# Performance work log

Measured on AMD Instinct MI355X. Metric: run time of the kernel, lower is better.

The kernel has to match this reference:

```python
import jax, jax.numpy as jnp
import numpy as np

B, TE, TD = 16, 400, 64
E, H = 256, 512
H2 = 2 * H  # 1024
V = 32000


def setup_inputs():
    key = jax.random.key(0)
    k = jax.random.split(key, 16)
    s = 0.05
    return {
        "encoder_inputs": jax.random.randint(k[0], (B, TE), 0, V),
        "decoder_inputs": jax.random.randint(k[1], (B, TD), 0, V),
        "ext_oov_sizes": jax.random.randint(k[2], (B,), 0, 10),
        "enc_idxes_on_ext_voc": jax.random.randint(k[3], (B, TE), 0, V),
        "h0": jnp.zeros((2, B, H), jnp.float32),
        "c0": jnp.zeros((2, B, H), jnp.float32),
        "emb": jax.random.normal(k[4], (V, E)) * 0.1,
        "Wih_f": jax.random.normal(k[5], (4 * H, E)) * s,
        "Whh_f": jax.random.normal(k[6], (4 * H, H)) * s,
        "b_f": jnp.zeros((4 * H,), jnp.float32),
        "Wih_b": jax.random.normal(k[7], (4 * H, E)) * s,
        "Whh_b": jax.random.normal(k[8], (4 * H, H)) * s,
        "b_b": jnp.zeros((4 * H,), jnp.float32),
        "Wih_d": jax.random.normal(k[9], (4 * H2, E + 2 * H2)) * s,
        "Whh_d": jax.random.normal(k[10], (4 * H2, H2)) * s,
        "b_d": jnp.zeros((4 * H2,), jnp.float32),
        "W_ea": jax.random.normal(k[11], (H2, H2)) * 0.006,
        "W_da": jax.random.normal(k[12], (H2, H2)) * 0.006,
        "W_v": jax.random.normal(k[13], (V, 3 * H2)) * s,
        "b_v": jnp.zeros((V,), jnp.float32),
    }


def lstm_cell(x, h, c, Wih, Whh, b):
    z = x @ Wih.T + h @ Whh.T + b
    i, f, g, o = jnp.split(z, 4, axis=-1)
    i, f, o = jax.nn.sigmoid(i), jax.nn.sigmoid(f), jax.nn.sigmoid(o)
    c2 = f * c + i * jnp.tanh(g)
    return o * jnp.tanh(c2), c2


def run_lstm(xs, h0, c0, Wih, Whh, b):
    # xs: [T, B, E]
    def step(carry, x):
        h, c = lstm_cell(x, carry[0], carry[1], Wih, Whh, b)
        return (h, c), h
    (h, c), hs = jax.lax.scan(step, (h0, c0), xs)
    return hs, h, c


def _forward(emb, Wih_f, Whh_f, b_f, Wih_b, Whh_b, b_b, Wih_d, Whh_d, b_d,
             W_ea, W_da, W_v, b_v, h0, c0, encoder_inputs, decoder_inputs):
    xs = emb[encoder_inputs].transpose(1, 0, 2)  # [TE, B, E]
    hs_f, hf, cf = run_lstm(xs, h0[0], c0[0], Wih_f, Whh_f, b_f)
    hs_b, hb, cb = run_lstm(xs[::-1], h0[1], c0[1], Wih_b, Whh_b, b_b)
    enc_out = jnp.concatenate([hs_f, hs_b[::-1]], axis=-1).transpose(1, 0, 2)  # [B, TE, 2H]
    h = jnp.concatenate([hf, hb], axis=-1)  # [B, 2H] (torch reshape of bi-dir last hidden)
    c = jnp.concatenate([cf, cb], axis=-1)
    dec_emb = emb[decoder_inputs].transpose(1, 0, 2)  # [TD, B, E]

    def step(carry, xs_t):
        h, c, accum, buf = carry
        i, emb_t = xs_t
        # intra-temporal encoder attention: exp scores normalized by past accumulation
        scores = jnp.einsum('bd,btd->bt', h @ W_ea, enc_out)  # [B, TE]
        exp_s = jnp.exp(scores)
        denom = jnp.where(i == 0, jnp.ones_like(accum), accum)
        ep = exp_s / denom
        attn = ep / jnp.sum(ep, axis=-1, keepdims=True)
        ctx_e = jnp.einsum('bt,btd->bd', attn, enc_out)
        # intra-decoder attention over previously produced hidden states (masked)
        dsc = jnp.einsum('bd,tbd->bt', h @ W_da, buf)  # [B, TD]
        dsc = jnp.where((jnp.arange(TD) < i)[None, :], dsc, -1e30)
        dw = jnp.where(i == 0, 0.0, jax.nn.softmax(dsc, axis=-1))
        ctx_d = jnp.einsum('bt,tbd->bd', dw, buf)
        x = jnp.concatenate([emb_t, ctx_e, ctx_d], axis=-1)  # [B, E+4H]
        h2, c2 = lstm_cell(x, h, c, Wih_d, Whh_d, b_d)
        buf2 = buf.at[i].set(h2)
        feat = jnp.concatenate([h2, ctx_e, ctx_d], axis=-1)  # [B, 6H]
        logd = jax.nn.log_softmax(feat @ W_v.T + b_v, axis=-1)
        return (h2, c2, accum + exp_s, buf2), logd

    carry0 = (h, c, jnp.zeros((B, TE), h.dtype), jnp.zeros((TD, B, H2), h.dtype))
    (h, c, _, _), logds = jax.lax.scan(step, carry0, (jnp.arange(TD), dec_emb))
    return logds.transpose(1, 0, 2), h[None], c[None]


def reference(encoder_inputs, decoder_inputs, ext_oov_sizes, enc_idxes_on_ext_voc,
              h0, c0, emb, Wih_f, Whh_f, b_f, Wih_b, Whh_b, b_b,
              Wih_d, Whh_d, b_d, W_ea, W_da, W_v, b_v):
    # ext_oov_sizes / enc_idxes_on_ext_voc are unused by forward (as in the torch source)
    return _forward(emb, Wih_f, Whh_f, b_f, Wih_b, Whh_b, b_b, Wih_d, Whh_d, b_d,
                    W_ea, W_da, W_v, b_v, h0, c0, encoder_inputs, decoder_inputs)
```

## Files before the change

kernel.cpp:

```cpp
#include <hip/hip_runtime.h>
#include <math.h>

#define B_  16
#define TE_ 400
#define TD_ 64
#define E_  256
#define H_  512
#define H2_ 1024
#define V_  32000

typedef __attribute__((ext_vector_type(4))) float f32x4;
typedef __attribute__((ext_vector_type(8))) short s16x8;
typedef __attribute__((ext_vector_type(8))) unsigned short u16x8;
typedef __attribute__((ext_vector_type(4))) unsigned short u16x4;

__device__ __forceinline__ float bf2f(unsigned short u){
  union { unsigned int i; float f; } v; v.i = ((unsigned int)u) << 16; return v.f;
}
__device__ __forceinline__ unsigned short f2bf(float f){
  union { float f; unsigned int i; } v; v.f = f;
  return (unsigned short)((v.i + 0x7fffu + ((v.i >> 16) & 1u)) >> 16);
}
__device__ __forceinline__ float sigmoidf_(float x){ return 1.f/(1.f + expf(-x)); }

__device__ __forceinline__ void gl_lds16(const void* gsrc, void* ldst){
  __builtin_amdgcn_global_load_lds(
      (const __attribute__((address_space(1))) unsigned int*)gsrc,
      (__attribute__((address_space(3))) unsigned int*)ldst, 16, 0, 0);
}

__device__ __forceinline__ void arrive8(unsigned* inst){
  __threadfence();
  __hip_atomic_fetch_add(inst + (blockIdx.x & 7u)*16, 1u, __ATOMIC_RELAXED, __HIP_MEMORY_SCOPE_AGENT);
}
__device__ __forceinline__ void poll8(unsigned* inst, unsigned target){
  int it = 0;
  for(;;){
    unsigned s = 0;
    #pragma unroll
    for (int k = 0; k < 8; ++k)
      s += __hip_atomic_load(inst + k*16, __ATOMIC_RELAXED, __HIP_MEMORY_SCOPE_AGENT);
    if (s >= target) break;
    if (it < 6) __builtin_amdgcn_s_sleep(1);
    else if (it < 24) __builtin_amdgcn_s_sleep(4);
    else __builtin_amdgcn_s_sleep(16);
    ++it;
  }
}

__global__ void k_init(unsigned* bars, float* ctxn, float* psumT){
  int gid = blockIdx.x*256 + threadIdx.x;
  if (gid < 81920) bars[gid] = 0u;
  if (gid < 32768) ctxn[gid] = 0.f;
  if (gid < 32) psumT[gid] = 0.f;
}

__global__ void k_gather(const float* __restrict__ emb, const int* __restrict__ idx,
                         unsigned short* __restrict__ out, int T){
  int wv = threadIdx.x >> 6, l = threadIdx.x & 63;
  int row = blockIdx.x*4 + wv;
  if (row >= T*B_) return;
  int t = row >> 4, b = row & 15;
  int tok = idx[b*T + t];
  float4 v = *(const float4*)(emb + (size_t)tok*E_ + l*4);
  u16x4 o; o[0]=f2bf(v.x); o[1]=f2bf(v.y); o[2]=f2bf(v.z); o[3]=f2bf(v.w);
  *(u16x4*)(out + (size_t)row*E_ + l*4) = o;
}

__global__ void k_prep_enc(const float* __restrict__ Wih_f, const float* __restrict__ Whh_f,
                           const float* __restrict__ Wih_b, const float* __restrict__ Whh_b,
                           unsigned short* __restrict__ Wenc){
  int it = blockIdx.x*256 + threadIdx.x;
  int dir = it / (2048*96); int rem = it % (2048*96);
  int pr = rem / 96; int kc = rem % 96; int k0 = kc*8;
  int g = pr >> 6, r = pr & 63, gate = r >> 4, ul = r & 15;
  int orig = gate*H_ + g*16 + ul;
  const float* Wih = dir ? Wih_b : Wih_f;
  const float* Whh = dir ? Whh_b : Whh_f;
  u16x8 o;
  #pragma unroll
  for (int e = 0; e < 8; ++e){
    int k = k0 + e;
    float v = (k < E_) ? Wih[(size_t)orig*E_ + k] : Whh[(size_t)orig*H_ + (k - E_)];
    o[e] = f2bf(v);
  }
  *(u16x8*)(Wenc + ((size_t)dir*2048 + pr)*768 + k0) = o;
}

__device__ __forceinline__ void prep_whext_item(int it, const float* __restrict__ Whh_d,
                                                const float* __restrict__ W_da,
                                                char* __restrict__ WhExt){
  if (it < 524288){
    int g = it >> 13; int rem = it & 8191;
    int kblk = rem >> 10; int rem2 = rem & 1023;
    int row = rem2 >> 4; int k8 = rem2 & 15;
    int gate = row >> 4, ul = row & 15;
    int orig = gate*H2_ + g*16 + ul;
    u16x8 o;
    #pragma unroll
    for (int e = 0; e < 8; ++e)
      o[e] = f2bf(Whh_d[(size_t)orig*H2_ + kblk*128 + k8*8 + e]);
    size_t off = (size_t)g*163840 + (size_t)kblk*20480 + (size_t)(row*256 + ((k8*16) ^ ((row&7)<<4)));
    *(u16x8*)(WhExt + off) = o;
  } else if (it < 655360){
    int qi = it - 524288;
    int g = qi >> 11; int rem = qi & 2047;
    int kblk = rem >> 8; int c2 = rem & 255;
    int wvv = c2 >> 6, rr = (c2 >> 2) & 15, c = c2 & 3;
    int row = g*16 + rr;
    u16x8 o;
    #pragma unroll
    for (int e = 0; e < 8; ++e)
      o[e] = f2bf(W_da[(size_t)row*H2_ + kblk*128 + wvv*32 + c*8 + e]);
    size_t off = (size_t)g*163840 + (size_t)kblk*20480 + 16384
               + (size_t)(wvv*1024 + rr*64 + ((c*16) ^ ((rr&3)<<4)));
    *(u16x8*)(WhExt + off) = o;
  }
}

__device__ __forceinline__ void prep_ctx_item(int it, const float* __restrict__ Wih_d,
                                              char* __restrict__ CtxW){
  int g = it >> 14; int rem = it & 16383;
  int kblk = rem >> 10; int rem2 = rem & 1023;
  int row = rem2 >> 4; int k8 = rem2 & 15;
  int gate = row >> 4, ul = row & 15;
  int orig = gate*H2_ + g*16 + ul;
  int k = 256 + kblk*128 + k8*8;
  u16x8 o;
  #pragma unroll
  for (int e = 0; e < 8; ++e)
    o[e] = f2bf(Wih_d[(size_t)orig*2304 + k + e]);
  size_t off = (size_t)g*262144 + (size_t)kblk*16384 + (size_t)(row*256 + ((k8*16) ^ ((row&7)<<4)));
  *(u16x8*)(CtxW + off) = o;
}

__global__ void k_prep_wihemb(const float* __restrict__ Wih_d, unsigned short* __restrict__ Wemb){
  int it = blockIdx.x*256 + threadIdx.x;
  int p = it >> 5; int k0 = (it & 31)*8;
  int g = p >> 6, gate = (p >> 4) & 3, ul = p & 15;
  int orig = gate*H2_ + g*16 + ul;
  u16x8 o;
  #pragma unroll
  for (int e = 0; e < 8; ++e)
    o[e] = f2bf(Wih_d[(size_t)orig*2304 + k0 + e]);
  *(u16x8*)(Wemb + (size_t)p*256 + k0) = o;
}

__global__ void __launch_bounds__(256, 2) k_zinit(
    const unsigned short* __restrict__ A,
    const unsigned short* __restrict__ Bw,
    const float* __restrict__ bd,
    float* __restrict__ Cz)
{
  __shared__ unsigned short Ab[128*72];
  __shared__ unsigned short Bt[128*72];
  int p = blockIdx.x;
  int mt = p >> 5, nt = p & 31;
  int m0 = mt*128, n0 = nt*128;
  int tid = threadIdx.x, wvv = tid>>6, l = tid&63;
  int wr = wvv>>1, wc = wvv&1;
  f32x4 zero4 = {0.f,0.f,0.f,0.f};
  f32x4 acc[4][4];
  #pragma unroll
  for (int a=0;a<4;++a){
    #pragma unroll
    for (int b=0;b<4;++b) acc[a][b] = zero4;
  }
  for (int k0 = 0; k0 < 256; k0 += 64){
    #pragma unroll
    for (int qq = 0; qq < 4; ++qq){
      int idx8 = (tid + qq*256)*8;
      int r = idx8 >> 6, k = idx8 & 63;
      *(u16x8*)(Ab + r*72 + k) = *(const u16x8*)(A + (size_t)(m0+r)*256 + k0 + k);
      *(u16x8*)(Bt + r*72 + k) = *(const u16x8*)(Bw + (size_t)(n0+r)*256 + k0 + k);
    }
    __syncthreads();
    #pragma unroll
    for (int ks = 0; ks < 2; ++ks){
      s16x8 af[4], bf[4];
      #pragma unroll
      for (int fi=0;fi<4;++fi)
        af[fi] = *(const s16x8*)(Ab + (wr*64+fi*16+(l&15))*72 + ks*32 + (l>>4)*8);
      #pragma unroll
      for (int fj=0;fj<4;++fj)
        bf[fj] = *(const s16x8*)(Bt + (wc*64+fj*16+(l&15))*72 + ks*32 + (l>>4)*8);
      #pragma unroll
      for (int fi=0;fi<4;++fi){
        #pragma unroll
        for (int fj=0;fj<4;++fj)
          acc[fi][fj] = __builtin_amdgcn_mfma_f32_16x16x32_bf16(af[fi], bf[fj], acc[fi][fj], 0,0,0);
      }
    }
    __syncthreads();
  }
  #pragma unroll
  for (int fj=0;fj<4;++fj){
    int col = n0 + wc*64 + fj*16 + (l&15);
    int orig = ((col>>4)&3)*H2_ + (col>>6)*16 + (col&15);
    float bias = bd[orig];
    #pragma unroll
    for (int fi=0;fi<4;++fi){
      #pragma unroll
      for (int j=0;j<4;++j){
        int row = m0 + wr*64 + fi*16 + (l>>4)*4 + j;
        Cz[(size_t)row*4096 + col] = acc[fi][fj][j] + bias;
      }
    }
  }
}

__global__ void __launch_bounds__(256, 2) k_zx(
    const unsigned short* __restrict__ xs,
    const unsigned short* __restrict__ Wenc,
    const float* __restrict__ b_f, const float* __restrict__ b_b,
    unsigned short* __restrict__ zx)
{
  __shared__ unsigned short Ab[128*72];
  __shared__ unsigned short Bt[128*72];
  int pblk = blockIdx.x;
  int dir = pblk / 800; int rem = pblk % 800;
  int mt = rem >> 4, nt = rem & 15;
  int m0 = mt*128, n0 = nt*128;
  int tid = threadIdx.x, wvv = tid>>6, l = tid&63;
  int wr = wvv>>1, wc = wvv&1;
  f32x4 zero4 = {0.f,0.f,0.f,0.f};
  f32x4 acc[4][4];
  #pragma unroll
  for (int a=0;a<4;++a){
    #pragma unroll
    for (int b=0;b<4;++b) acc[a][b] = zero4;
  }
  for (int k0 = 0; k0 < 256; k0 += 64){
    #pragma unroll
    for (int qq = 0; qq < 4; ++qq){
      int idx8 = (tid + qq*256)*8;
      int r = idx8 >> 6, k = idx8 & 63;
      *(u16x8*)(Ab + r*72 + k) = *(const u16x8*)(xs + (size_t)(m0+r)*256 + k0 + k);
      *(u16x8*)(Bt + r*72 + k) = *(const u16x8*)(Wenc + ((size_t)dir*2048 + n0+r)*768 + k0 + k);
    }
    __syncthreads();
    #pragma unroll
    for (int ks = 0; ks < 2; ++ks){
      s16x8 af[4], bf[4];
      #pragma unroll
      for (int fi=0;fi<4;++fi)
        af[fi] = *(const s16x8*)(Ab + (wr*64+fi*16+(l&15))*72 + ks*32 + (l>>4)*8);
      #pragma unroll
      for (int fj=0;fj<4;++fj)
        bf[fj] = *(const s16x8*)(Bt + (wc*64+fj*16+(l&15))*72 + ks*32 + (l>>4)*8);
      #pragma unroll
      for (int fi=0;fi<4;++fi){
        #pragma unroll
        for (int fj=0;fj<4;++fj)
          acc[fi][fj] = __builtin_amdgcn_mfma_f32_16x16x32_bf16(af[fi], bf[fj], acc[fi][fj], 0,0,0);
      }
    }
    __syncthreads();
  }
  const float* bsrc = dir ? b_b : b_f;
  #pragma unroll
  for (int fj=0;fj<4;++fj){
    int col = n0 + wc*64 + fj*16 + (l&15);
    float bias = bsrc[((col>>4)&3)*512 + (col>>6)*16 + (col&15)];
    #pragma unroll
    for (int fi=0;fi<4;++fi){
      #pragma unroll
      for (int j=0;j<4;++j){
        int row = m0 + wr*64 + fi*16 + (l>>4)*4 + j;
        zx[((size_t)dir*6400 + row)*2048 + col] = f2bf(acc[fi][fj][j] + bias);
      }
    }
  }
}

__global__ void __launch_bounds__(256, 2) k_penc(
    const unsigned short* __restrict__ enc,
    const float* __restrict__ Wea,
    unsigned short* __restrict__ P)
{
  __shared__ unsigned short Ab[128*72];
  __shared__ unsigned short Bt[128*72];
  int p = blockIdx.x;
  int mt = p >> 3, nt = p & 7;
  int m0 = mt*128, n0 = nt*128;
  int tid = threadIdx.x, wvv = tid>>6, l = tid&63;
  int wr = wvv>>1, wc = wvv&1;
  f32x4 zero4 = {0.f,0.f,0.f,0.f};
  f32x4 acc[4][4];
  #pragma unroll
  for (int a=0;a<4;++a){
    #pragma unroll
    for (int b=0;b<4;++b) acc[a][b] = zero4;
  }
  for (int k0 = 0; k0 < 1024; k0 += 64){
    #pragma unroll
    for (int qq = 0; qq < 4; ++qq){
      int idx8 = (tid + qq*256)*8;
      int r = idx8 >> 6, k = idx8 & 63;
      *(u16x8*)(Ab + r*72 + k) = *(const u16x8*)(enc + (size_t)(m0+r)*1024 + k0 + k);
    }
    #pragma unroll
    for (int qq = 0; qq < 4; ++qq){
      int idx8 = (tid + qq*256)*8;
      int r = idx8 >> 6, k = idx8 & 63;
      const float* src = Wea + (size_t)(n0+r)*1024 + k0 + k;
      float4 v0 = *(const float4*)src;
      float4 v1 = *(const float4*)(src+4);
      u16x8 o;
      o[0]=f2bf(v0.x); o[1]=f2bf(v0.y); o[2]=f2bf(v0.z); o[3]=f2bf(v0.w);
      o[4]=f2bf(v1.x); o[5]=f2bf(v1.y); o[6]=f2bf(v1.z); o[7]=f2bf(v1.w);
      *(u16x8*)(Bt + r*72 + k) = o;
    }
    __syncthreads();
    #pragma unroll
    for (int ks = 0; ks < 2; ++ks){
      s16x8 af[4], bf[4];
      #pragma unroll
      for (int fi=0;fi<4;++fi)
        af[fi] = *(const s16x8*)(Ab + (wr*64+fi*16+(l&15))*72 + ks*32 + (l>>4)*8);
      #pragma unroll
      for (int fj=0;fj<4;++fj)
        bf[fj] = *(const s16x8*)(Bt + (wc*64+fj*16+(l&15))*72 + ks*32 + (l>>4)*8);
      #pragma unroll
      for (int fi=0;fi<4;++fi){
        #pragma unroll
        for (int fj=0;fj<4;++fj)
          acc[fi][fj] = __builtin_amdgcn_mfma_f32_16x16x32_bf16(af[fi], bf[fj], acc[fi][fj], 0,0,0);
      }
    }
    __syncthreads();
  }
  #pragma unroll
  for (int fj=0;fj<4;++fj){
    int col = n0 + wc*64 + fj*16 + (l&15);
    #pragma unroll
    for (int fi=0;fi<4;++fi){
      #pragma unroll
      for (int j=0;j<4;++j){
        int row = m0 + wr*64 + fi*16 + (l>>4)*4 + j;
        P[(size_t)row*1024 + col] = f2bf(acc[fi][fj][j]);
      }
    }
  }
}

__global__ void __launch_bounds__(256, 1) k_encoder(
    const unsigned short* __restrict__ zx,
    const unsigned short* __restrict__ Wenc,
    const float* __restrict__ h0, const float* __restrict__ c0,
    unsigned short* __restrict__ enc_out,
    unsigned short* __restrict__ hbuf,
    float* __restrict__ h0dec, float* __restrict__ c0dec,
    unsigned* __restrict__ bars,
    const float* __restrict__ Whh_d, const float* __restrict__ W_da,
    const float* __restrict__ Wih_d,
    char* __restrict__ WhExt, char* __restrict__ CtxW)
{
  extern __shared__ char smem[];
  int tid = threadIdx.x;
  int w = blockIdx.x;
  if (w >= 64){
    int base = (w - 64)*256 + tid;
    for (int it = base; it < 655360; it += 36864) prep_whext_item(it, Whh_d, W_da, WhExt);
    for (int it = base; it < 1048576; it += 36864) prep_ctx_item(it, Wih_d, CtxW);
    return;
  }
  unsigned short* Wt = (unsigned short*)smem;
  unsigned short* At = Wt + 64*520;
  float* zl = (float*)(At + 16*520);
  int dir = w >> 5, g = w & 31;
  int wv = tid >> 6, l = tid & 63;
  {
    const unsigned short* Wsrc = Wenc + ((size_t)dir*2048 + g*64)*768 + 256;
    int r = tid >> 2, s = tid & 3;
    for (int c = 0; c < 16; ++c)
      *(u16x8*)(Wt + r*520 + s*128 + c*8) = *(const u16x8*)(Wsrc + (size_t)r*768 + s*128 + c*8);
  }
  int bb = tid >> 4, ul = tid & 15;
  float creg = c0[((size_t)dir*16 + bb)*H_ + g*16 + ul];
  int kchunk = (l >> 4) * 8;
  f32x4 zero4 = { 0.f, 0.f, 0.f, 0.f };
  {
    int r = tid >> 4, s = tid & 15;
    for (int e = 0; e < 32; ++e)
      At[r*520 + s*32 + e] = f2bf(h0[((size_t)dir*16 + r)*H_ + s*32 + e]);
  }
  int tg0 = dir ? (TE_-1) : 0;
  const unsigned short* zrow = zx + ((size_t)dir*6400 + (size_t)tg0*16 + (l>>4)*4)*2048 + g*64 + wv*16 + (l&15);
  f32x4 a0cur;
  a0cur[0]=bf2f(zrow[0]); a0cur[1]=bf2f(zrow[2048]); a0cur[2]=bf2f(zrow[4096]); a0cur[3]=bf2f(zrow[6144]);
  __syncthreads();
  for (int t = 0; t < TE_; ++t){
    int tg = dir ? (TE_-1 - t) : t;
    f32x4 acc0 = a0cur, acc1 = zero4;
    const unsigned short* brow = Wt + (wv*16 + (l&15))*520 + kchunk;
    const unsigned short* ap   = At + (l&15)*520 + kchunk;
    #pragma unroll
    for (int ks = 0; ks < 16; ++ks){
      s16x8 afr = *(const s16x8*)(ap + ks*32);
      s16x8 bfr = *(const s16x8*)(brow + ks*32);
      if (ks & 1) acc1 = __builtin_amdgcn_mfma_f32_16x16x32_bf16(afr, bfr, acc1, 0, 0, 0);
      else        acc0 = __builtin_amdgcn_mfma_f32_16x16x32_bf16(afr, bfr, acc0, 0, 0, 0);
    }
    f32x4 acc = acc0 + acc1;
    #pragma unroll
    for (int j = 0; j < 4; ++j)
      zl[wv*256 + ((l>>4)*4 + j)*16 + (l&15)] = acc[j];
    __syncthreads();
    float zi = zl[0*256 + bb*16 + ul];
    float zf = zl[1*256 + bb*16 + ul];
    float zg = zl[2*256 + bb*16 + ul];
    float zo = zl[3*256 + bb*16 + ul];
    float iv = sigmoidf_(zi), fv = sigmoidf_(zf), gv = tanhf(zg), ov = sigmoidf_(zo);
    float cc = fv*creg + iv*gv;
    float hh = ov * tanhf(cc);
    creg = cc;
    int u = g*16 + ul;
    unsigned short hb = f2bf(hh);
    hbuf[((size_t)dir*2 + ((t+1)&1))*(16*H_) + bb*H_ + u] = hb;
    enc_out[((size_t)bb*TE_ + tg)*H2_ + dir*H_ + u] = hb;
    if (t == TE_-1){
      h0dec[(size_t)bb*H2_ + dir*H_ + u] = hh;
      c0dec[(size_t)bb*H2_ + dir*H_ + u] = cc;
    }
    unsigned* cnt = bars + (size_t)(dir*400 + t)*64;
    __syncthreads();
    if (tid == 0){
      __threadfence();
      __hip_atomic_fetch_add(cnt + (g&3)*16, 1u, __ATOMIC_RELAXED, __HIP_MEMORY_SCOPE_AGENT);
    }
    if (t+1 < TE_){
      int tg2 = dir ? (TE_-2 - t) : (t+1);
      const unsigned short* zr2 = zx + ((size_t)dir*6400 + (size_t)tg2*16 + (l>>4)*4)*2048 + g*64 + wv*16 + (l&15);
      a0cur[0]=bf2f(zr2[0]); a0cur[1]=bf2f(zr2[2048]); a0cur[2]=bf2f(zr2[4096]); a0cur[3]=bf2f(zr2[6144]);
    }
    if (tid == 0){
      int it = 0;
      for(;;){
        unsigned s_ = 0;
        #pragma unroll
        for (int k2 = 0; k2 < 4; ++k2)
          s_ += __hip_atomic_load(cnt + k2*16, __ATOMIC_RELAXED, __HIP_MEMORY_SCOPE_AGENT);
        if (s_ >= 32) break;
        if (it < 6) __builtin_amdgcn_s_sleep(1);
        else __builtin_amdgcn_s_sleep(4);
        ++it;
      }
      __threadfence();
    }
    __syncthreads();
    if (t+1 < TE_){
      int r = tid >> 4, s = tid & 15;
      const unsigned short* hsrc = hbuf + ((size_t)dir*2 + ((t+1)&1))*(16*H_) + r*H_ + s*32;
      for (int c = 0; c < 4; ++c)
        *(u16x8*)(At + r*520 + s*32 + c*8) = *(const u16x8*)(hsrc + c*8);
    }
    __syncthreads();
  }
}

__global__ void k_dec_init(const float* __restrict__ h0dec, unsigned short* __restrict__ hreg){
  int gid = blockIdx.x*256 + threadIdx.x;
  if (gid < 16384) hreg[gid] = f2bf(h0dec[gid]);
}

__device__ __forceinline__ void issueA(const char* gA, char* BbA, int wv, int l, int kblk, int buf){
  const char* gsrc = gA + (size_t)kblk*20480;
  char* lb = BbA + buf*20480;
  #pragma unroll
  for (int q = 0; q < 4; ++q)
    gl_lds16(gsrc + wv*4096 + q*1024 + (size_t)l*16, lb + wv*4096 + q*1024);
  gl_lds16(gsrc + 16384 + wv*1024 + (size_t)l*16, lb + 16384 + wv*1024);
}
__device__ __forceinline__ void issueC(const char* gC, char* BbC, int wv, int l, int kblk, int buf){
  const char* gsrc = gC + (size_t)kblk*16384;
  char* lb = BbC + buf*16384;
  #pragma unroll
  for (int q = 0; q < 4; ++q)
    gl_lds16(gsrc + wv*4096 + q*1024 + (size_t)l*16, lb + wv*4096 + q*1024);
}

__global__ void __launch_bounds__(256, 1) k_decoder(
  const char* __restrict__ WhExt,
  const char* __restrict__ CtxW,
  const float* __restrict__ zinit,
  const unsigned short* __restrict__ Penc,
  const unsigned short* __restrict__ enc_out,
  const float* __restrict__ c0dec,
  unsigned short* __restrict__ hreg,
  unsigned short* __restrict__ xbuf,
  float* __restrict__ ctxn,
  float* __restrict__ psumT,
  unsigned short* __restrict__ vbuf,
  unsigned short* __restrict__ bufh,
  unsigned short* __restrict__ Av,
  float* __restrict__ outHC,
  unsigned* __restrict__ bars)
{
  extern __shared__ char smem[];
  int tid = threadIdx.x, w = blockIdx.x;
  int wv = tid >> 6, l = tid & 63;
  unsigned* dbase = bars + 51200;

  unsigned short* Atc = (unsigned short*)smem;
  unsigned short* Ah  = (unsigned short*)smem;
  char* BbA = smem + 66560;
  char* BbC = smem + 128000;
  float* zq = (float*)(smem + 66560);
  float* zl = (float*)(smem + 128000);
  unsigned short* encL = (unsigned short*)smem;
  float* epL  = (float*)(smem + 103424);
  float* accL = (float*)(smem + 103680);
  float* dscL = (float*)smem;

  bool isZ = (w < 64);
  bool isE = (w >= 64 && w < 192);
  int eb = 0, ec = 0;
  if (isE){ eb = (w-64) >> 3; ec = (w-64) & 7; }
  int db = w - 192;

  if (isE){
    for (int rr = 0; rr < 50; ++rr){
      const unsigned short* src = enc_out + ((size_t)eb*TE_ + ec*50 + rr)*H2_;
      *(u16x4*)(encL + rr*1032 + tid*4) = *(const u16x4*)(src + tid*4);
    }
    if (tid < 50) accL[tid] = 0.f;
    __syncthreads();
  }
  float creg = 0.f;
  int bb = tid >> 4, ul = tid & 15;
  const char* gA = WhExt + (size_t)w*163840;
  const char* gC = CtxW + (size_t)w*262144;
  f32x4 acc0, acc1;

  for (int i = 0; i < TD_; ++i){
    int p = i & 1;
    unsigned* barM = dbase + (size_t)(i*3+0)*128;
    unsigned* barA = dbase + (size_t)(i*3+1)*128;
    unsigned* barB = dbase + (size_t)(i*3+2)*128;

    if (isZ){
      ctxn[(p^1)*16384 + w*256 + tid] = 0.f;
      if (w == 0 && tid < 16) psumT[(p^1)*16 + tid] = 0.f;
      const float* zsrc = zinit + ((size_t)i*16 + (l>>4)*4)*4096 + w*64 + wv*16 + (l&15);
      f32x4 a0i; a0i[0]=zsrc[0]; a0i[1]=zsrc[4096]; a0i[2]=zsrc[8192]; a0i[3]=zsrc[12288];
      issueA(gA, BbA, wv, l, 0, 0);
      issueA(gA, BbA, wv, l, 1, 1);
      {
        int r = tid >> 4, s = tid & 15;
        const unsigned short* hsrc = hreg + p*16384 + r*H2_ + s*64;
        for (int c = 0; c < 8; ++c)
          *(u16x8*)(Ah + r*1032 + s*64 + c*8) = *(const u16x8*)(hsrc + c*8);
      }
      __syncthreads();
      acc0 = a0i;
      f32x4 z4 = {0.f,0.f,0.f,0.f};
      acc1 = z4;
      f32x4 accv = z4;
      int swz = ((l&7)<<4);
      for (int kblk = 0; kblk < 8; ++kblk){
        int buf = kblk % 3;
        if (kblk + 2 < 8) issueA(gA, BbA, wv, l, kblk+2, (kblk+2)%3);
        if (kblk < 6)       asm volatile("s_waitcnt vmcnt(10)" ::: "memory");
        else if (kblk == 6) asm volatile("s_waitcnt vmcnt(5)" ::: "memory");
        else                asm volatile("s_waitcnt vmcnt(0)" ::: "memory");
        const unsigned short* ap = Ah + (l&15)*1032 + kblk*128 + (l>>4)*8;
        const char* Bz = BbA + buf*20480 + wv*4096;
        #pragma unroll
        for (int ks = 0; ks < 4; ++ks){
          int k8 = ks*4 + (l>>4);
          s16x8 afr = *(const s16x8*)(ap + ks*32);
          s16x8 bfr = *(const s16x8*)(Bz + (l&15)*256 + ((k8*16) ^ swz));
          if (ks & 1) acc1 = __builtin_amdgcn_mfma_f32_16x16x32_bf16(afr, bfr, acc1, 0,0,0);
          else        acc0 = __builtin_amdgcn_mfma_f32_16x16x32_bf16(afr, bfr, acc0, 0,0,0);
        }
        s16x8 afq = *(const s16x8*)(Ah + (l&15)*1032 + kblk*128 + wv*32 + (l>>4)*8);
        s16x8 bfv = *(const s16x8*)(BbA + buf*20480 + 16384 + wv*1024 + (l&15)*64 + ((((l>>4)*16)) ^ ((l&3)<<4)));
        accv = __builtin_amdgcn_mfma_f32_16x16x32_bf16(afq, bfv, accv, 0,0,0);
      }
      __syncthreads();
      #pragma unroll
      for (int j = 0; j < 4; ++j)
        zq[wv*256 + ((l>>4)*4+j)*16 + (l&15)] = accv[j];
      __syncthreads();
      if (i > 0){
        float vv = zq[0*256+bb*16+ul] + zq[1*256+bb*16+ul] + zq[2*256+bb*16+ul] + zq[3*256+bb*16+ul];
        vbuf[((size_t)(i-1)*16 + bb)*H2_ + w*16 + ul] = f2bf(vv);
      }
      __syncthreads();
      if (tid == 0) arrive8(barM);
      issueC(gC, BbC, wv, l, 0, 0);
      issueC(gC, BbC, wv, l, 1, 1);
      if (tid == 0){ poll8(barA, 144); __threadfence(); }
      __syncthreads();
      {
        int r = tid >> 4, s = tid & 15;
        float inv = 1.f / psumT[p*16 + r];
        const float* cn = ctxn + p*16384 + (size_t)r*1024 + s*64;
        for (int c8 = 0; c8 < 8; ++c8){
          float4 v0 = *(const float4*)(cn + c8*8);
          float4 v1 = *(const float4*)(cn + c8*8 + 4);
          u16x8 o;
          o[0]=f2bf(v0.x*inv); o[1]=f2bf(v0.y*inv); o[2]=f2bf(v0.z*inv); o[3]=f2bf(v0.w*inv);
          o[4]=f2bf(v1.x*inv); o[5]=f2bf(v1.y*inv); o[6]=f2bf(v1.z*inv); o[7]=f2bf(v1.w*inv);
          *(u16x8*)(Atc + r*2056 + s*64 + c8*8) = o;
        }
        const unsigned short* xd = xbuf + (size_t)r*1024 + s*64;
        for (int c8 = 0; c8 < 8; ++c8)
          *(u16x8*)(Atc + r*2056 + 1024 + s*64 + c8*8) = *(const u16x8*)(xd + c8*8);
      }
      {
        float val = ctxn[p*16384 + (size_t)bb*1024 + w*16 + ul] / psumT[p*16 + bb];
        Av[((size_t)bb*TD_ + i)*3072 + 1024 + w*16 + ul] = f2bf(val);
      }
      __syncthreads();
      for (int k = 0; k < 16; ++k){
        if (k < 15) asm volatile("s_waitcnt vmcnt(4)" ::: "memory");
        else        asm volatile("s_waitcnt vmcnt(0)" ::: "memory");
        const unsigned short* ap = Atc + (l&15)*2056 + k*128 + (l>>4)*8;
        const char* Bz = BbC + (k&1)*16384 + wv*4096;
        #pragma unroll
        for (int ks = 0; ks < 4; ++ks){
          int k8 = ks*4 + (l>>4);
          s16x8 afr = *(const s16x8*)(ap + ks*32);
          s16x8 bfr = *(const s16x8*)(Bz + (l&15)*256 + ((k8*16) ^ swz));
          if (ks & 1) acc1 = __builtin_amdgcn_mfma_f32_16x16x32_bf16(afr, bfr, acc1, 0,0,0);
          else        acc0 = __builtin_amdgcn_mfma_f32_16x16x32_bf16(afr, bfr, acc0, 0,0,0);
        }
        if (k + 2 < 16) issueC(gC, BbC, wv, l, k+2, k&1);
      }
      __syncthreads();
      f32x4 acc = acc0 + acc1;
      #pragma unroll
      for (int j = 0; j < 4; ++j)
        zl[wv*256 + ((l>>4)*4+j)*16 + (l&15)] = acc[j];
      __syncthreads();
      float zi = zl[0*256 + bb*16 + ul];
      float zf = zl[1*256 + bb*16 + ul];
      float zg = zl[2*256 + bb*16 + ul];
      float zo = zl[3*256 + bb*16 + ul];
      if (i == 0) creg = c0dec[(size_t)bb*H2_ + w*16 + ul];
      float iv = sigmoidf_(zi), fv = sigmoidf_(zf), gv = tanhf(zg), ov = sigmoidf_(zo);
      float cc = fv*creg + iv*gv;
      float hh = ov*tanhf(cc);
      creg = cc;
      int u = w*16 + ul;
      unsigned short hb2 = f2bf(hh);
      hreg[((i+1)&1)*16384 + (size_t)bb*H2_ + u] = hb2;
      Av[((size_t)bb*TD_ + i)*3072 + u] = hb2;
      bufh[((size_t)i*16 + bb)*H2_ + u] = hb2;
      if (i == TD_-1){
        outHC[(size_t)bb*H2_ + u] = hh;
        outHC[16384 + (size_t)bb*H2_ + u] = cc;
      }
      __syncthreads();
      if (tid == 0){ arrive8(barB); poll8(barB, 64); __threadfence(); }
      __syncthreads();
    } else if (isE){
      const unsigned short* hb_ = hreg + p*16384 + eb*H2_ + l*16;
      u16x8 hv0 = *(const u16x8*)hb_;
      u16x8 hv1 = *(const u16x8*)(hb_ + 8);
      float hf[16];
      #pragma unroll
      for (int c = 0; c < 8; ++c){ hf[c] = bf2f(hv0[c]); hf[8+c] = bf2f(hv1[c]); }
      for (int rr = wv; rr < 50; rr += 4){
        const unsigned short* pr = Penc + ((size_t)(eb*TE_ + ec*50 + rr))*H2_ + l*16;
        u16x8 p0 = *(const u16x8*)pr;
        u16x8 p1 = *(const u16x8*)(pr + 8);
        float sc = 0.f;
        #pragma unroll
        for (int c = 0; c < 8; ++c) sc += hf[c]*bf2f(p0[c]);
        #pragma unroll
        for (int c = 0; c < 8; ++c) sc += hf[8+c]*bf2f(p1[c]);
        #pragma unroll
        for (int o = 1; o < 64; o <<= 1) sc += __shfl_xor(sc, o);
        if (l == 0){
          float es = expf(sc);
          float aold = accL[rr];
          float denom = (i == 0) ? 1.f : aold;
          accL[rr] = aold + es;
          epL[rr] = es / denom;
        }
      }
      __syncthreads();
      float tot = 0.f;
      for (int rr = 0; rr < 50; ++rr) tot += epL[rr];
      float a0=0.f,a1=0.f,a2=0.f,a3=0.f;
      for (int rr = 0; rr < 50; ++rr){
        float wgt = epL[rr];
        u16x4 ev = *(const u16x4*)(encL + rr*1032 + tid*4);
        a0 += wgt*bf2f(ev[0]); a1 += wgt*bf2f(ev[1]); a2 += wgt*bf2f(ev[2]); a3 += wgt*bf2f(ev[3]);
      }
      float* dst = ctxn + p*16384 + (size_t)eb*1024 + tid*4;
      atomicAdd(dst+0, a0); atomicAdd(dst+1, a1); atomicAdd(dst+2, a2); atomicAdd(dst+3, a3);
      if (tid == 0) atomicAdd(psumT + p*16 + eb, tot);
      __syncthreads();
      if (tid == 0){ arrive8(barA); poll8(barB, 64); __threadfence(); }
      __syncthreads();
    } else {
      int col = tid*4;
      if (i == 0){
        u16x4 z4v = {0,0,0,0};
        *(u16x4*)(xbuf + (size_t)db*1024 + col) = z4v;
        *(u16x4*)(Av + ((size_t)db*TD_ + i)*3072 + 2048 + col) = z4v;
      } else {
        if (tid == 0){ poll8(barM, 64); __threadfence(); }
        __syncthreads();
        const unsigned short* hq = hreg + p*16384 + db*H2_ + l*16;
        u16x8 h0v = *(const u16x8*)hq;
        u16x8 h1v = *(const u16x8*)(hq + 8);
        float qf[16];
        #pragma unroll
        for (int c = 0; c < 8; ++c){ qf[c] = bf2f(h0v[c]); qf[8+c] = bf2f(h1v[c]); }
        for (int tp = wv; tp < i; tp += 4){
          const unsigned short* vr = vbuf + ((size_t)tp*16 + db)*H2_ + l*16;
          u16x8 e0 = *(const u16x8*)vr;
          u16x8 e1 = *(const u16x8*)(vr + 8);
          float sc = 0.f;
          #pragma unroll
          for (int c = 0; c < 8; ++c) sc += qf[c]*bf2f(e0[c]);
          #pragma unroll
          for (int c = 0; c < 8; ++c) sc += qf[8+c]*bf2f(e1[c]);
          #pragma unroll
          for (int o = 1; o < 64; o <<= 1) sc += __shfl_xor(sc, o);
          if (l == 0) dscL[tp] = sc;
        }
        __syncthreads();
        float scv = (l < i) ? dscL[l] : -1e30f;
        float m = scv;
        #pragma unroll
        for (int o = 1; o < 64; o <<= 1) m = fmaxf(m, __shfl_xor(m, o));
        float e = (l < i) ? expf(scv - m) : 0.f;
        float ssum = e;
        #pragma unroll
        for (int o = 1; o < 64; o <<= 1) ssum += __shfl_xor(ssum, o);
        float wgt = e / ssum;
        float c0_=0.f,c1_=0.f,c2_=0.f,c3_=0.f;
        for (int tp = 0; tp < i; ++tp){
          float wt = __shfl(wgt, tp);
          u16x4 hv = *(const u16x4*)(bufh + ((size_t)tp*16 + db)*H2_ + col);
          c0_ += wt*bf2f(hv[0]); c1_ += wt*bf2f(hv[1]); c2_ += wt*bf2f(hv[2]); c3_ += wt*bf2f(hv[3]);
        }
        u16x4 o4; o4[0]=f2bf(c0_); o4[1]=f2bf(c1_); o4[2]=f2bf(c2_); o4[3]=f2bf(c3_);
        *(u16x4*)(xbuf + (size_t)db*1024 + col) = o4;
        *(u16x4*)(Av + ((size_t)db*TD_ + i)*3072 + 2048 + col) = o4;
      }
      __syncthreads();
      if (tid == 0){ arrive8(barA); poll8(barB, 64); __threadfence(); }
      __syncthreads();
    }
  }
}

__global__ void __launch_bounds__(256, 2) k_vocab_gemm(
    const unsigned short* __restrict__ Av,
    const float* __restrict__ Wv,
    const float* __restrict__ bv,
    float* __restrict__ out)
{
  __shared__ unsigned short Ab[128*72];
  __shared__ unsigned short Bt[128*72];
  int p = blockIdx.x;
  int mt = (p>>3)&7, nt = (p&7) + 8*(p>>6);
  if (nt >= 250) return;
  int m0 = mt*128, n0 = nt*128;
  int tid = threadIdx.x, wvv = tid>>6, l = tid&63;
  int wr = wvv>>1, wc = wvv&1;
  f32x4 zero4 = {0.f,0.f,0.f,0.f};
  f32x4 acc[4][4];
  #pragma unroll
  for (int a=0;a<4;++a){
    #pragma unroll
    for (int b=0;b<4;++b) acc[a][b] = zero4;
  }
  for (int k0 = 0; k0 < 3072; k0 += 64){
    #pragma unroll
    for (int qq = 0; qq < 4; ++qq){
      int idx8 = (tid + qq*256)*8;
      int r = idx8 >> 6, k = idx8 & 63;
      *(u16x8*)(Ab + r*72 + k) = *(const u16x8*)(Av + (size_t)(m0+r)*3072 + k0 + k);
    }
    #pragma unroll
    for (int qq = 0; qq < 4; ++qq){
      int idx8 = (tid + qq*256)*8;
      int r = idx8 >> 6, k = idx8 & 63;
      const float* src = Wv + (size_t)(n0+r)*3072 + k0 + k;
      float4 v0 = *(const float4*)src;
      float4 v1 = *(const float4*)(src+4);
      u16x8 o;
      o[0]=f2bf(v0.x); o[1]=f2bf(v0.y); o[2]=f2bf(v0.z); o[3]=f2bf(v0.w);
      o[4]=f2bf(v1.x); o[5]=f2bf(v1.y); o[6]=f2bf(v1.z); o[7]=f2bf(v1.w);
      *(u16x8*)(Bt + r*72 + k) = o;
    }
    __syncthreads();
    #pragma unroll
    for (int ks = 0; ks < 2; ++ks){
      s16x8 af[4], bf[4];
      #pragma unroll
      for (int fi=0;fi<4;++fi)
        af[fi] = *(const s16x8*)(Ab + (wr*64+fi*16+(l&15))*72 + ks*32 + (l>>4)*8);
      #pragma unroll
      for (int fj=0;fj<4;++fj)
        bf[fj] = *(const s16x8*)(Bt + (wc*64+fj*16+(l&15))*72 + ks*32 + (l>>4)*8);
      #pragma unroll
      for (int fi=0;fi<4;++fi){
        #pragma unroll
        for (int fj=0;fj<4;++fj)
          acc[fi][fj] = __builtin_amdgcn_mfma_f32_16x16x32_bf16(af[fi], bf[fj], acc[fi][fj], 0,0,0);
      }
    }
    __syncthreads();
  }
  #pragma unroll
  for (int fj=0;fj<4;++fj){
    int col = n0 + wc*64 + fj*16 + (l&15);
    float bias = bv[col];
    #pragma unroll
    for (int fi=0;fi<4;++fi){
      #pragma unroll
      for (int j=0;j<4;++j){
        int row = m0 + wr*64 + fi*16 + (l>>4)*4 + j;
        out[(size_t)row*V_ + col] = acc[fi][fj][j] + bias;
      }
    }
  }
}

__global__ void k_logsoftmax(float* __restrict__ out){
  int row = blockIdx.x;
  float* x = out + (size_t)row*V_;
  int tid = threadIdx.x;
  __shared__ float red[64];
  float m = -1e30f;
  for (int c = tid; c < V_; c += 256) m = fmaxf(m, x[c]);
  #pragma unroll
  for (int o=1;o<64;o<<=1) m = fmaxf(m, __shfl_xor(m,o));
  if ((tid&63)==0) red[tid>>6] = m;
  __syncthreads();
  m = fmaxf(fmaxf(red[0],red[1]), fmaxf(red[2],red[3]));
  float s = 0.f;
  for (int c = tid; c < V_; c += 256) s += expf(x[c]-m);
  #pragma unroll
  for (int o=1;o<64;o<<=1) s += __shfl_xor(s,o);
  if ((tid&63)==0) red[8 + (tid>>6)] = s;
  __syncthreads();
  s = red[8]+red[9]+red[10]+red[11];
  float lse = m + logf(s);
  for (int c = tid; c < V_; c += 256) x[c] = x[c] - lse;
}

extern "C" void kernel_launch(void* const* d_in, const int* in_sizes, int n_in,
                              void* d_out, int out_size, void* d_ws, size_t ws_size,
                              hipStream_t stream){
  (void)in_sizes; (void)n_in; (void)out_size; (void)ws_size;
  const int*   enc_in = (const int*)d_in[0];
  const int*   dec_in = (const int*)d_in[1];
  const float* h0   = (const float*)d_in[4];
  const float* c0   = (const float*)d_in[5];
  const float* emb  = (const float*)d_in[6];
  const float* Wih_f= (const float*)d_in[7];
  const float* Whh_f= (const float*)d_in[8];
  const float* b_f  = (const float*)d_in[9];
  const float* Wih_b= (const float*)d_in[10];
  const float* Whh_b= (const float*)d_in[11];
  const float* b_b  = (const float*)d_in[12];
  const float* Wih_d= (const float*)d_in[13];
  const float* Whh_d= (const float*)d_in[14];
  const float* b_d  = (const float*)d_in[15];
  const float* W_ea = (const float*)d_in[16];
  const float* W_da = (const float*)d_in[17];
  const float* W_v  = (const float*)d_in[18];
  const float* b_v  = (const float*)d_in[19];
  float* out = (float*)d_out;
  char* ws = (char*)d_ws;

  size_t o_bars   = 0;
  size_t o_ctxn   = 327680;
  size_t o_psumT  = o_ctxn + 131072;
  size_t o_xs     = o_psumT + 256;
  size_t o_decemb = o_xs + (size_t)6400*256*2;
  size_t o_Wenc   = o_decemb + (size_t)1024*256*2;
  size_t o_WhExt  = o_Wenc + (size_t)2*2048*768*2;
  size_t o_CtxW   = o_WhExt + (size_t)64*163840;
  size_t o_Wemb   = o_CtxW + (size_t)64*262144;
  size_t o_zinit  = o_Wemb + (size_t)4096*256*2;
  size_t o_zx     = o_zinit + (size_t)1024*4096*4;
  size_t o_enc    = o_zx + (size_t)2*6400*2048*2;
  size_t o_Penc   = o_enc + (size_t)16*400*1024*2;
  size_t o_hbuf   = o_Penc + (size_t)16*400*1024*2;
  size_t o_h0dec  = o_hbuf + (size_t)2*2*16*512*2;
  size_t o_c0dec  = o_h0dec + (size_t)16*1024*4;
  size_t o_hreg   = o_c0dec + (size_t)16*1024*4;
  size_t o_xbuf   = o_hreg + (size_t)2*16*1024*2;
  size_t o_vbuf   = o_xbuf + (size_t)16*1024*2;
  size_t o_bufh   = o_vbuf + (size_t)64*16*1024*2;
  size_t o_Av     = o_bufh + (size_t)64*16*1024*2;

  unsigned* bars        = (unsigned*)(ws + o_bars);
  float* ctxn           = (float*)(ws + o_ctxn);
  float* psumT          = (float*)(ws + o_psumT);
  unsigned short* xs    = (unsigned short*)(ws + o_xs);
  unsigned short* decemb= (unsigned short*)(ws + o_decemb);
  unsigned short* Wenc  = (unsigned short*)(ws + o_Wenc);
  char* WhExt           = ws + o_WhExt;
  char* CtxW            = ws + o_CtxW;
  unsigned short* Wemb  = (unsigned short*)(ws + o_Wemb);
  float* zinit          = (float*)(ws + o_zinit);
  unsigned short* zx    = (unsigned short*)(ws + o_zx);
  unsigned short* encO  = (unsigned short*)(ws + o_enc);
  unsigned short* Penc  = (unsigned short*)(ws + o_Penc);
  unsigned short* hbuf  = (unsigned short*)(ws + o_hbuf);
  float* h0dec          = (float*)(ws + o_h0dec);
  float* c0dec          = (float*)(ws + o_c0dec);
  unsigned short* hreg  = (unsigned short*)(ws + o_hreg);
  unsigned short* xbuf  = (unsigned short*)(ws + o_xbuf);
  unsigned short* vbuf  = (unsigned short*)(ws + o_vbuf);
  unsigned short* bufh  = (unsigned short*)(ws + o_bufh);
  unsigned short* Av    = (unsigned short*)(ws + o_Av);

  hipFuncSetAttribute((const void*)k_encoder, hipFuncAttributeMaxDynamicSharedMemorySize, 90000);
  hipFuncSetAttribute((const void*)k_decoder, hipFuncAttributeMaxDynamicSharedMemorySize, 160768);

  k_init<<<320, 256, 0, stream>>>(bars, ctxn, psumT);
  k_gather<<<1600, 256, 0, stream>>>(emb, enc_in, xs, TE_);
  k_gather<<<256, 256, 0, stream>>>(emb, dec_in, decemb, TD_);
  k_prep_enc<<<1536, 256, 0, stream>>>(Wih_f, Whh_f, Wih_b, Whh_b, Wenc);
  k_prep_wihemb<<<512, 256, 0, stream>>>(Wih_d, Wemb);
  k_zinit<<<256, 256, 0, stream>>>(decemb, Wemb, b_d, zinit);
  k_zx<<<1600, 256, 0, stream>>>(xs, Wenc, b_f, b_b, zx);
  k_encoder<<<208, 256, 87296, stream>>>(zx, Wenc, h0, c0, encO, hbuf, h0dec, c0dec, bars,
                                         Whh_d, W_da, Wih_d, WhExt, CtxW);
  k_penc<<<400, 256, 0, stream>>>(encO, W_ea, Penc);
  k_dec_init<<<64, 256, 0, stream>>>(h0dec, hreg);
  k_decoder<<<208, 256, 160768, stream>>>(WhExt, CtxW, zinit, Penc, encO, c0dec,
                                          hreg, xbuf, ctxn, psumT, vbuf, bufh, Av,
                                          out + (size_t)32768000, bars);
  k_vocab_gemm<<<2048, 256, 0, stream>>>(Av, W_v, b_v, out);
  k_logsoftmax<<<1024, 256, 0, stream>>>(out);
}
```

Baseline: 5.538 ms.

## Deepen decoder ctx-weight prefetch, hoist A prefetch across barrier, warm L2, relayout barriers

The decoder's context-weight stream now uses a four-deep buffer that borrows the A-weight LDS slots, where it was double-buffered before. The next step's A-weight prefetch is issued before the end-of-step barrier poll instead of at the start of the step. Idle attention blocks read the Z-blocks' weight slices while waiting, to keep them warm in L2. Barrier counters are re-laid out so each per-block-group counter array is contiguous, which needs a larger init region and a shifted workspace offset. The aim is to hide weight-load latency and barrier wait time in the serial decoder loop, at the cost of extra memory traffic and LDS slot aliasing that must stay race-free.

```diff
diff --git a/kernel.cpp b/kernel.cpp
--- a/kernel.cpp
+++ b/kernel.cpp
@@ -29,28 +29,29 @@
       (__attribute__((address_space(3))) unsigned int*)ldst, 16, 0, 0);
 }
 
-__device__ __forceinline__ void arrive8(unsigned* inst){
+__device__ __forceinline__ void d_arrive(unsigned* bars, int inst){
   __threadfence();
-  __hip_atomic_fetch_add(inst + (blockIdx.x & 7u)*16, 1u, __ATOMIC_RELAXED, __HIP_MEMORY_SCOPE_AGENT);
-}
-__device__ __forceinline__ void poll8(unsigned* inst, unsigned target){
+  __hip_atomic_fetch_add(bars + (blockIdx.x & 7u)*4096 + inst*16, 1u, __ATOMIC_RELAXED, __HIP_MEMORY_SCOPE_AGENT);
+}
+__device__ __forceinline__ void d_poll(unsigned* bars, int inst, unsigned tgt){
   int it = 0;
   for(;;){
     unsigned s = 0;
     #pragma unroll
     for (int k = 0; k < 8; ++k)
-      s += __hip_atomic_load(inst + k*16, __ATOMIC_RELAXED, __HIP_MEMORY_SCOPE_AGENT);
-    if (s >= target) break;
+      s += __hip_atomic_load(bars + k*4096 + inst*16, __ATOMIC_RELAXED, __HIP_MEMORY_SCOPE_AGENT);
+    if (s >= tgt) break;
     if (it < 6) __builtin_amdgcn_s_sleep(1);
     else if (it < 24) __builtin_amdgcn_s_sleep(4);
     else __builtin_amdgcn_s_sleep(16);
     ++it;
   }
+  __threadfence();
 }
 
 __global__ void k_init(unsigned* bars, float* ctxn, float* psumT){
   int gid = blockIdx.x*256 + threadIdx.x;
-  if (gid < 81920) bars[gid] = 0u;
+  if (gid < 99328) bars[gid] = 0u;
   if (gid < 32768) ctxn[gid] = 0.f;
   if (gid < 32) psumT[gid] = 0.f;
 }
@@ -370,6 +371,7 @@
   float* zl = (float*)(At + 16*520);
   int dir = w >> 5, g = w & 31;
   int wv = tid >> 6, l = tid & 63;
+  unsigned* ebars = bars + 32768;
   {
     const unsigned short* Wsrc = Wenc + ((size_t)dir*2048 + g*64)*768 + 256;
     int r = tid >> 2, s = tid & 3;
@@ -423,11 +425,11 @@
       h0dec[(size_t)bb*H2_ + dir*H_ + u] = hh;
       c0dec[(size_t)bb*H2_ + dir*H_ + u] = cc;
     }
-    unsigned* cnt = bars + (size_t)(dir*400 + t)*64;
+    int inst = dir*400 + t;
     __syncthreads();
     if (tid == 0){
       __threadfence();
-      __hip_atomic_fetch_add(cnt + (g&3)*16, 1u, __ATOMIC_RELAXED, __HIP_MEMORY_SCOPE_AGENT);
+      __hip_atomic_fetch_add(ebars + (g&3)*16384 + inst*16, 1u, __ATOMIC_RELAXED, __HIP_MEMORY_SCOPE_AGENT);
     }
     if (t+1 < TE_){
       int tg2 = dir ? (TE_-2 - t) : (t+1);
@@ -440,7 +442,7 @@
         unsigned s_ = 0;
         #pragma unroll
         for (int k2 = 0; k2 < 4; ++k2)
-          s_ += __hip_atomic_load(cnt + k2*16, __ATOMIC_RELAXED, __HIP_MEMORY_SCOPE_AGENT);
+          s_ += __hip_atomic_load(ebars + k2*16384 + inst*16, __ATOMIC_RELAXED, __HIP_MEMORY_SCOPE_AGENT);
         if (s_ >= 32) break;
         if (it < 6) __builtin_amdgcn_s_sleep(1);
         else __builtin_amdgcn_s_sleep(4);
@@ -472,9 +474,12 @@
     gl_lds16(gsrc + wv*4096 + q*1024 + (size_t)l*16, lb + wv*4096 + q*1024);
   gl_lds16(gsrc + 16384 + wv*1024 + (size_t)l*16, lb + 16384 + wv*1024);
 }
-__device__ __forceinline__ void issueC(const char* gC, char* BbC, int wv, int l, int kblk, int buf){
+__device__ __forceinline__ char* cslot(char* BbA, char* BbC, int s){
+  if (s < 2) return BbC + s*16384;
+  return BbA + (s-2)*20480;
+}
+__device__ __forceinline__ void issueC(const char* gC, char* lb, int wv, int l, int kblk){
   const char* gsrc = gC + (size_t)kblk*16384;
-  char* lb = BbC + buf*16384;
   #pragma unroll
   for (int q = 0; q < 4; ++q)
     gl_lds16(gsrc + wv*4096 + q*1024 + (size_t)l*16, lb + wv*4096 + q*1024);
@@ -500,7 +505,6 @@
   extern __shared__ char smem[];
   int tid = threadIdx.x, w = blockIdx.x;
   int wv = tid >> 6, l = tid & 63;
-  unsigned* dbase = bars + 51200;
 
   unsigned short* Atc = (unsigned short*)smem;
   unsigned short* Ah  = (unsigned short*)smem;
@@ -531,21 +535,28 @@
   int bb = tid >> 4, ul = tid & 15;
   const char* gA = WhExt + (size_t)w*163840;
   const char* gC = CtxW + (size_t)w*262144;
+  const char* warmbase = 0; int warmhalf4 = 0;
+  if (isE){
+    int j = w - 64;
+    if (j < 64){ warmbase = WhExt + (size_t)j*163840; warmhalf4 = 5120; }
+    else       { warmbase = CtxW + (size_t)(j-64)*262144; warmhalf4 = 8192; }
+  }
   f32x4 acc0, acc1;
+
+  if (isZ){
+    issueA(gA, BbA, wv, l, 0, 0);
+    issueA(gA, BbA, wv, l, 1, 1);
+  }
 
   for (int i = 0; i < TD_; ++i){
     int p = i & 1;
-    unsigned* barM = dbase + (size_t)(i*3+0)*128;
-    unsigned* barA = dbase + (size_t)(i*3+1)*128;
-    unsigned* barB = dbase + (size_t)(i*3+2)*128;
+    int iM = i*3, iAb = i*3+1, iBb = i*3+2;
 
     if (isZ){
       ctxn[(p^1)*16384 + w*256 + tid] = 0.f;
       if (w == 0 && tid < 16) psumT[(p^1)*16 + tid] = 0.f;
       const float* zsrc = zinit + ((size_t)i*16 + (l>>4)*4)*4096 + w*64 + wv*16 + (l&15);
       f32x4 a0i; a0i[0]=zsrc[0]; a0i[1]=zsrc[4096]; a0i[2]=zsrc[8192]; a0i[3]=zsrc[12288];
-      issueA(gA, BbA, wv, l, 0, 0);
-      issueA(gA, BbA, wv, l, 1, 1);
       {
         int r = tid >> 4, s = tid & 15;
         const unsigned short* hsrc = hreg + p*16384 + r*H2_ + s*64;
@@ -588,10 +599,12 @@
         vbuf[((size_t)(i-1)*16 + bb)*H2_ + w*16 + ul] = f2bf(vv);
       }
       __syncthreads();
-      if (tid == 0) arrive8(barM);
-      issueC(gC, BbC, wv, l, 0, 0);
-      issueC(gC, BbC, wv, l, 1, 1);
-      if (tid == 0){ poll8(barA, 144); __threadfence(); }
+      if (tid == 0) d_arrive(bars, iM);
+      issueC(gC, cslot(BbA, BbC, 0), wv, l, 0);
+      issueC(gC, cslot(BbA, BbC, 1), wv, l, 1);
+      issueC(gC, cslot(BbA, BbC, 2), wv, l, 2);
+      issueC(gC, cslot(BbA, BbC, 3), wv, l, 3);
+      if (tid == 0) d_poll(bars, iAb, 144);
       __syncthreads();
       {
         int r = tid >> 4, s = tid & 15;
@@ -614,20 +627,24 @@
         Av[((size_t)bb*TD_ + i)*3072 + 1024 + w*16 + ul] = f2bf(val);
       }
       __syncthreads();
+      int swz2 = ((l&7)<<4);
       for (int k = 0; k < 16; ++k){
-        if (k < 15) asm volatile("s_waitcnt vmcnt(4)" ::: "memory");
-        else        asm volatile("s_waitcnt vmcnt(0)" ::: "memory");
+        int rem = 15 - k;
+        if (rem >= 3)      asm volatile("s_waitcnt vmcnt(12)" ::: "memory");
+        else if (rem == 2) asm volatile("s_waitcnt vmcnt(8)" ::: "memory");
+        else if (rem == 1) asm volatile("s_waitcnt vmcnt(4)" ::: "memory");
+        else               asm volatile("s_waitcnt vmcnt(0)" ::: "memory");
         const unsigned short* ap = Atc + (l&15)*2056 + k*128 + (l>>4)*8;
-        const char* Bz = BbC + (k&1)*16384 + wv*4096;
+        const char* Bz = cslot(BbA, BbC, k&3) + wv*4096;
         #pragma unroll
         for (int ks = 0; ks < 4; ++ks){
           int k8 = ks*4 + (l>>4);
           s16x8 afr = *(const s16x8*)(ap + ks*32);
-          s16x8 bfr = *(const s16x8*)(Bz + (l&15)*256 + ((k8*16) ^ swz));
+          s16x8 bfr = *(const s16x8*)(Bz + (l&15)*256 + ((k8*16) ^ swz2));
           if (ks & 1) acc1 = __builtin_amdgcn_mfma_f32_16x16x32_bf16(afr, bfr, acc1, 0,0,0);
           else        acc0 = __builtin_amdgcn_mfma_f32_16x16x32_bf16(afr, bfr, acc0, 0,0,0);
         }
-        if (k + 2 < 16) issueC(gC, BbC, wv, l, k+2, k&1);
+        if (k + 4 < 16) issueC(gC, cslot(BbA, BbC, (k+4)&3), wv, l, k+4);
       }
       __syncthreads();
       f32x4 acc = acc0 + acc1;
@@ -654,7 +671,12 @@
         outHC[16384 + (size_t)bb*H2_ + u] = cc;
       }
       __syncthreads();
-      if (tid == 0){ arrive8(barB); poll8(barB, 64); __threadfence(); }
+      if (tid == 0) d_arrive(bars, iBb);
+      if (i + 1 < TD_){
+        issueA(gA, BbA, wv, l, 0, 0);
+        issueA(gA, BbA, wv, l, 1, 1);
+      }
+      if (tid == 0) d_poll(bars, iBb, 64);
       __syncthreads();
     } else if (isE){
       const unsigned short* hb_ = hreg + p*16384 + eb*H2_ + l*16;
@@ -695,7 +717,17 @@
       atomicAdd(dst+0, a0); atomicAdd(dst+1, a1); atomicAdd(dst+2, a2); atomicAdd(dst+3, a3);
       if (tid == 0) atomicAdd(psumT + p*16 + eb, tot);
       __syncthreads();
-      if (tid == 0){ arrive8(barA); poll8(barB, 64); __threadfence(); }
+      if (tid == 0) d_arrive(bars, iAb);
+      {
+        const unsigned* wb = (const unsigned*)(warmbase + (size_t)(i & 1)*warmhalf4*16);
+        unsigned accw = 0;
+        for (int o = tid; o < warmhalf4; o += 256){
+          uint4 v = *(const uint4*)(wb + o*4);
+          accw ^= v.x ^ v.y ^ v.z ^ v.w;
+        }
+        asm volatile("" :: "v"(accw));
+      }
+      if (tid == 0) d_poll(bars, iBb, 64);
       __syncthreads();
     } else {
       int col = tid*4;
@@ -704,7 +736,7 @@
         *(u16x4*)(xbuf + (size_t)db*1024 + col) = z4v;
         *(u16x4*)(Av + ((size_t)db*TD_ + i)*3072 + 2048 + col) = z4v;
       } else {
-        if (tid == 0){ poll8(barM, 64); __threadfence(); }
+        if (tid == 0) d_poll(bars, iM, 64);
         __syncthreads();
         const unsigned short* hq = hreg + p*16384 + db*H2_ + l*16;
         u16x8 h0v = *(const u16x8*)hq;
@@ -746,7 +778,7 @@
         *(u16x4*)(Av + ((size_t)db*TD_ + i)*3072 + 2048 + col) = o4;
       }
       __syncthreads();
-      if (tid == 0){ arrive8(barA); poll8(barB, 64); __threadfence(); }
+      if (tid == 0){ d_arrive(bars, iAb); d_poll(bars, iBb, 64); }
       __syncthreads();
     }
   }
@@ -875,7 +907,7 @@
   char* ws = (char*)d_ws;
 
   size_t o_bars   = 0;
-  size_t o_ctxn   = 327680;
+  size_t o_ctxn   = 397312;
   size_t o_psumT  = o_ctxn + 131072;
   size_t o_xs     = o_psumT + 256;
   size_t o_decemb = o_xs + (size_t)6400*256*2;
@@ -921,7 +953,7 @@
   hipFuncSetAttribute((const void*)k_encoder, hipFuncAttributeMaxDynamicSharedMemorySize, 90000);
   hipFuncSetAttribute((const void*)k_decoder, hipFuncAttributeMaxDynamicSharedMemorySize, 160768);
 
-  k_init<<<320, 256, 0, stream>>>(bars, ctxn, psumT);
+  k_init<<<392, 256, 0, stream>>>(bars, ctxn, psumT);
   k_gather<<<1600, 256, 0, stream>>>(emb, enc_in, xs, TE_);
   k_gather<<<256, 256, 0, stream>>>(emb, dec_in, decemb, TD_);
   k_prep_enc<<<1536, 256, 0, stream>>>(Wih_f, Whh_f, Wih_b, Whh_b, Wenc);
```

Measured after the change: 5.337 ms. -3.6%, faster.
